# Performance work log

Hardware: AMD Instinct MI355X
Metric: run time of the kernel (lower is better)

Reference implementation:

```python
import jax, jax.numpy as jnp
import numpy as np

ATTN_MASK_VALUE = -1e10
N, D_IN, D_HEAD, D_OUT = 8192, 1024, 128, 1024


def setup_inputs() -> dict:
    key = jax.random.key(0)
    k_x, k_wqkv, k_bqkv, k_wo, k_bo = jax.random.split(key, 5)
    x = jax.random.normal(k_x, (N, D_IN), dtype=jnp.float32)
    # flax Dense default: lecun_normal kernel, zeros bias; use scaled normal for test
    w_qkv = jax.random.normal(k_wqkv, (D_IN, 3 * D_HEAD), dtype=jnp.float32) / np.sqrt(D_IN)
    b_qkv = jnp.zeros((3 * D_HEAD,), dtype=jnp.float32)
    w_out = jax.random.normal(k_wo, (D_HEAD, D_OUT), dtype=jnp.float32) / np.sqrt(D_HEAD)
    b_out = jnp.zeros((D_OUT,), dtype=jnp.float32)
    return {"x": x, "w_qkv": w_qkv, "b_qkv": b_qkv, "w_out": w_out, "b_out": b_out}


def reference(x, w_qkv, b_qkv, w_out, b_out):
    n = x.shape[0]
    scale = D_HEAD ** (-0.5)
    qkv = x @ w_qkv + b_qkv                      # [n, 3*dh]
    q, k, v = jnp.split(qkv, 3, axis=-1)         # each [n, dh]
    sim = jnp.einsum('id,jd->ij', q, k) * scale  # [n, n]
    mask = jnp.triu(jnp.ones((n, n), dtype=bool), 1)
    sim = jnp.where(mask, ATTN_MASK_VALUE, sim)
    attn = jax.nn.softmax(sim, axis=-1)
    out = jnp.einsum('ij,jd->id', attn, v)       # [n, dh]
    return out @ w_out + b_out                   # [n, d_out]
```

## Files before the change

kernel.cpp:

```cpp
#include <hip/hip_runtime.h>
#include <stdint.h>

typedef __attribute__((ext_vector_type(4))) float f32x4;
typedef __attribute__((ext_vector_type(8))) __bf16 bf16x8;

#define MFMA16(a, b, c) __builtin_amdgcn_mfma_f32_16x16x32_bf16(a, b, c, 0, 0, 0)
#define GLOAD16(g, l)                                                              \
  __builtin_amdgcn_global_load_lds(                                                \
      (const __attribute__((address_space(1))) unsigned int*)(g),                  \
      (__attribute__((address_space(3))) unsigned int*)(l), 16, 0, 0)
#define EXP2F(x) __builtin_amdgcn_exp2f(x)

static __device__ __forceinline__ unsigned short f2b(float f) {
  unsigned int u = __float_as_uint(f);
  u += 0x7fff + ((u >> 16) & 1);
  return (unsigned short)(u >> 16);
}
static __device__ __forceinline__ float b2f(unsigned short h) {
  unsigned int u = ((unsigned int)h) << 16;
  return __uint_as_float(u);
}
static __device__ __forceinline__ unsigned int cvt_pk_bf16(float a, float b) {
  unsigned int r;
  asm("v_cvt_pk_bf16_f32 %0, %1, %2" : "=v"(r) : "v"(a), "v"(b));
  return r;
}

#define NROWS 8192
#define DIN   1024
#define DH    128
#define DOUT  1024

__global__ void k_convert(const float* __restrict__ x, const float* __restrict__ wqkv,
                          const float* __restrict__ wout,
                          unsigned short* __restrict__ xb,
                          unsigned short* __restrict__ wqkvT, unsigned short* __restrict__ woutT) {
  const int bid = blockIdx.x;
  const int tid = threadIdx.x;
  if (bid < 8192) {
    int i = (bid * 256 + tid) * 4;
    float4 v = *reinterpret_cast<const float4*>(x + i);
    ushort4 h;
    h.x = f2b(v.x); h.y = f2b(v.y); h.z = f2b(v.z); h.w = f2b(v.w);
    *reinterpret_cast<ushort4*>(xb + i) = h;
    return;
  }
  __shared__ float t[64][65];
  const int wb = bid - 8192;
  const float* src;
  unsigned short* dst;
  int k0, n0, sstride, dstride;
  if (wb < 96) {
    int kt = wb / 6, nt = wb % 6;
    k0 = kt * 64; n0 = nt * 64;
    src = wqkv; sstride = 384; dst = wqkvT; dstride = 1024;
  } else {
    int b2 = wb - 96;
    int kt = b2 & 1, nt = b2 >> 1;
    k0 = kt * 64; n0 = nt * 64;
    src = wout; sstride = 1024; dst = woutT; dstride = 128;
  }
  const int r = tid >> 4, c4 = (tid & 15) * 4;
#pragma unroll
  for (int j = 0; j < 4; ++j) {
    int rr = r + j * 16;
    float4 v = *reinterpret_cast<const float4*>(src + (size_t)(k0 + rr) * sstride + n0 + c4);
    t[rr][c4 + 0] = v.x; t[rr][c4 + 1] = v.y; t[rr][c4 + 2] = v.z; t[rr][c4 + 3] = v.w;
  }
  __syncthreads();
#pragma unroll
  for (int j = 0; j < 4; ++j) {
    int rn = r + j * 16;
    ushort4 h;
    h.x = f2b(t[c4 + 0][rn]); h.y = f2b(t[c4 + 1][rn]);
    h.z = f2b(t[c4 + 2][rn]); h.w = f2b(t[c4 + 3][rn]);
    *reinterpret_cast<ushort4*>(dst + (size_t)(n0 + rn) * dstride + k0 + c4) = h;
  }
}

__launch_bounds__(256, 2)
__global__ void k_qkv_gemm(const unsigned short* __restrict__ xb, const unsigned short* __restrict__ wT,
                           const float* __restrict__ bqkv,
                           unsigned short* __restrict__ Qb, unsigned short* __restrict__ Kb,
                           unsigned short* __restrict__ Vb) {
  const int hb = blockIdx.x;
  const int xcd = hb & 7, jj = hb >> 3;
  const int tau = xcd * 48 + jj;
  const int bn = tau % 6, bm = tau / 6;
  const int tid = threadIdx.x;
  const int lane = tid & 63, w = tid >> 6;
  const int l15 = lane & 15, g = lane >> 4;
  const int wm = (w >> 1) * 64, wn = (w & 1) * 32;
  const int row0 = bm * 128, col0 = bn * 64;

  __shared__ __align__(16) char Ash[2][16384];
  __shared__ __align__(16) char Bsh[2][8192];

  f32x4 acc[4][2] = {};

#define QKV_STAGE(k0, buf)                                                          \
  {                                                                                 \
    _Pragma("unroll")                                                               \
    for (int j2 = 0; j2 < 4; ++j2) {                                                \
      int idx = j2 * 256 + tid;                                                     \
      int r = idx >> 3, gg = idx & 7, sgg = gg ^ (r & 7);                           \
      GLOAD16(xb + (size_t)(row0 + r) * DIN + (k0) + sgg * 8, Ash[buf] + idx * 16); \
    }                                                                               \
    _Pragma("unroll")                                                               \
    for (int j2 = 0; j2 < 2; ++j2) {                                                \
      int idx = j2 * 256 + tid;                                                     \
      int r = idx >> 3, gg = idx & 7, sgg = gg ^ (r & 7);                           \
      GLOAD16(wT + (size_t)(col0 + r) * DIN + (k0) + sgg * 8, Bsh[buf] + idx * 16); \
    }                                                                               \
  }

  QKV_STAGE(0, 0);
  __syncthreads();
  int cur = 0;
  for (int k0 = 0; k0 < DIN; k0 += 64) {
    if (k0 + 64 < DIN) QKV_STAGE(k0 + 64, cur ^ 1);
#pragma unroll
    for (int ksl = 0; ksl < 2; ++ksl) {
      bf16x8 af[4], bfr[2];
#pragma unroll
      for (int i = 0; i < 4; ++i) {
        int r = wm + i * 16 + l15;
        int ba = r * 128 + ksl * 64 + g * 16;
        af[i] = *reinterpret_cast<bf16x8*>(Ash[cur] + (ba ^ ((r & 7) << 4)));
      }
#pragma unroll
      for (int jn = 0; jn < 2; ++jn) {
        int n = wn + jn * 16 + l15;
        int bb = n * 128 + ksl * 64 + g * 16;
        bfr[jn] = *reinterpret_cast<bf16x8*>(Bsh[cur] + (bb ^ ((n & 7) << 4)));
      }
#pragma unroll
      for (int i = 0; i < 4; ++i)
#pragma unroll
        for (int jn = 0; jn < 2; ++jn)
          acc[i][jn] = MFMA16(af[i], bfr[jn], acc[i][jn]);
    }
    __syncthreads();
    cur ^= 1;
  }

  const int which = col0 >> 7;
  const int inner = col0 & 127;
  unsigned short* outb = (which == 0) ? Qb : (which == 1 ? Kb : Vb);
#pragma unroll
  for (int i = 0; i < 4; ++i)
#pragma unroll
    for (int jn = 0; jn < 2; ++jn)
#pragma unroll
      for (int r = 0; r < 4; ++r) {
        int grow = row0 + wm + i * 16 + g * 4 + r;
        int lcol = wn + jn * 16 + l15;
        float vv = acc[i][jn][r] + bqkv[col0 + lcol];
        outb[(size_t)grow * DH + inner + lcol] = f2b(vv);
      }
}

__global__ void k_transpose_v(const unsigned short* __restrict__ V, unsigned short* __restrict__ VT) {
  __shared__ __align__(16) unsigned short t[64 * 128];
  const int b = blockIdx.x;
  const int tid = threadIdx.x;
  const int kv0 = b * 64;
#pragma unroll
  for (int j = 0; j < 4; ++j) {
    int c = j * 256 + tid;
    int r = c >> 4, cc = (c & 15) * 8;
    uint4 v = *reinterpret_cast<const uint4*>(V + (size_t)(kv0 + r) * DH + cc);
    int col = (cc + ((r >> 3) & 7) * 8) & 127;
    *reinterpret_cast<uint4*>(&t[r * 128 + col]) = v;
  }
  __syncthreads();
#pragma unroll
  for (int j = 0; j < 4; ++j) {
    int c = j * 256 + tid;
    int d = c >> 3, kk = (c & 7) * 8;
    unsigned short tmp[8];
#pragma unroll
    for (int e = 0; e < 8; ++e) {
      int r = kk + e;
      int col = (d + ((r >> 3) & 7) * 8) & 127;
      tmp[e] = t[r * 128 + col];
    }
    *reinterpret_cast<uint4*>(VT + (size_t)d * NROWS + kv0 + kk) = *reinterpret_cast<uint4*>(tmp);
  }
}

__launch_bounds__(256, 2)
__global__ void k_flash(const unsigned short* __restrict__ Q, const unsigned short* __restrict__ Kg,
                        const unsigned short* __restrict__ VT,
                        unsigned short* __restrict__ Opart, float* __restrict__ MLpart, int LQ) {
  const int ci = blockIdx.x;
  const int t = (int)(gridDim.y - 1) - (int)blockIdx.y;
  const int Jq = 1 << LQ;
  if (ci * Jq > t) return;
  const int qb = t << 7;
  const int ks = ci * (Jq << 7);
  const int ke = min(ks + (Jq << 7), qb + 128);
  const int nsteps = (ke - ks) >> 6;

  const int a = t >> LQ, b = t & (Jq - 1);
  const int slot = t + ((Jq * a * (a - 1)) >> 1) + a * b + ci;

  const int tid = threadIdx.x;
  const int lane = tid & 63, w = tid >> 6;
  const int l15 = lane & 15, g = lane >> 4;

  __shared__ __align__(16) char Ksh[2][16384];
  __shared__ __align__(16) char Vsh[2][16384];
  __shared__ __align__(16) char Psh[4][4096];

  const int qr0 = qb + w * 16 + l15;
  const int qr1 = qr0 + 64;
  bf16x8 qf0[4], qf1[4];
#pragma unroll
  for (int d = 0; d < 4; ++d) {
    qf0[d] = *reinterpret_cast<const bf16x8*>(Q + (size_t)qr0 * DH + d * 32 + g * 8);
    qf1[d] = *reinterpret_cast<const bf16x8*>(Q + (size_t)qr1 * DH + d * 32 + g * 8);
  }

  f32x4 acco0[8] = {}, acco1[8] = {};
  float m0 = -1e30f, l0 = 0.f, m1 = -1e30f, l1 = 0.f;
  const float c2 = 0.08838834764831843f * 1.4426950408889634f;

#define FL_STAGE(kv0, buf)                                                            \
  {                                                                                   \
    _Pragma("unroll")                                                                 \
    for (int j2 = 0; j2 < 4; ++j2) {                                                  \
      int idx = j2 * 256 + tid;                                                       \
      int r = idx >> 4, gg = idx & 15, sgg = gg ^ (r & 7);                            \
      GLOAD16(Kg + (size_t)((kv0) + r) * DH + sgg * 8, Ksh[buf] + idx * 16);          \
    }                                                                                 \
    _Pragma("unroll")                                                                 \
    for (int j2 = 0; j2 < 4; ++j2) {                                                  \
      int idx = j2 * 256 + tid;                                                       \
      int d = idx >> 3, gg = idx & 7, sgg = gg ^ (d & 7);                             \
      GLOAD16(VT + (size_t)d * NROWS + (kv0) + sgg * 8, Vsh[buf] + idx * 16);         \
    }                                                                                 \
  }

  char* Pw = Psh[w];

  FL_STAGE(ks, 0);
  __syncthreads();
  int cur = 0;

  for (int s = 0; s < nsteps; ++s) {
    const int kv0 = ks + (s << 6);
    if (s + 1 < nsteps) FL_STAGE(kv0 + 64, cur ^ 1);
    const bool act0 = (kv0 < qb + 64);

    f32x4 accs0[4] = {}, accs1[4] = {};
    __builtin_amdgcn_s_setprio(1);
    if (act0) {
#pragma unroll
      for (int jc = 0; jc < 4; ++jc)
#pragma unroll
        for (int d = 0; d < 4; ++d) {
          int r = jc * 16 + l15;
          int byte = r * 256 + d * 64 + g * 16; byte ^= (r & 7) << 4;
          bf16x8 kf = *reinterpret_cast<bf16x8*>(Ksh[cur] + byte);
          accs1[jc] = MFMA16(kf, qf1[d], accs1[jc]);
          accs0[jc] = MFMA16(kf, qf0[d], accs0[jc]);
        }
    } else {
#pragma unroll
      for (int jc = 0; jc < 4; ++jc)
#pragma unroll
        for (int d = 0; d < 4; ++d) {
          int r = jc * 16 + l15;
          int byte = r * 256 + d * 64 + g * 16; byte ^= (r & 7) << 4;
          bf16x8 kf = *reinterpret_cast<bf16x8*>(Ksh[cur] + byte);
          accs1[jc] = MFMA16(kf, qf1[d], accs1[jc]);
        }
    }
    __builtin_amdgcn_s_setprio(0);

#define SOFTMAX_PW(ACCS, ACCO, M, L, QROW, ROWBASE)                                   \
    {                                                                                 \
      float p[4][4];                                                                  \
      float mx = -3e38f;                                                              \
      _Pragma("unroll")                                                               \
      for (int jc = 0; jc < 4; ++jc)                                                  \
        _Pragma("unroll")                                                             \
        for (int r = 0; r < 4; ++r) {                                                 \
          float sv = ACCS[jc][r] * c2;                                                \
          int kk = kv0 + jc * 16 + (g << 2) + r;                                      \
          sv = (kk <= (QROW)) ? sv : -3e38f;                                          \
          p[jc][r] = sv;                                                              \
          mx = fmaxf(mx, sv);                                                         \
        }                                                                             \
      mx = fmaxf(mx, __shfl_xor(mx, 16));                                             \
      mx = fmaxf(mx, __shfl_xor(mx, 32));                                             \
      if (!__all(mx <= M + 8.f)) {             \
        float mnew = fmaxf(M, mx);                                                    \
        float fac = EXP2F(M - mnew);                                                  \
        L *= fac;                                                                     \
        M = mnew;                                                                     \
        _Pragma("unroll")                                                             \
        for (int dc = 0; dc < 8; ++dc)                                                \
          _Pragma("unroll")                                                           \
          for (int r = 0; r < 4; ++r) ACCO[dc][r] *= fac;                             \
      }                                                                               \
      float ps = 0.f;                                                                 \
      _Pragma("unroll")                                                               \
      for (int jc = 0; jc < 4; ++jc)                                                  \
        _Pragma("unroll")                                                             \
        for (int r = 0; r < 4; ++r) {                                                 \
          float e = EXP2F(p[jc][r] - M);                                              \
          p[jc][r] = e; ps += e;                                                      \
        }                                                                             \
      ps += __shfl_xor(ps, 16);                                                       \
      ps += __shfl_xor(ps, 32);                                                       \
      L += ps;                                                                        \
      int rq = (ROWBASE) + l15;                                                       \
      _Pragma("unroll")                                                               \
      for (int jc = 0; jc < 4; ++jc) {                                                \
        uint2 pb;                                                                     \
        pb.x = cvt_pk_bf16(p[jc][0], p[jc][1]);                                       \
        pb.y = cvt_pk_bf16(p[jc][2], p[jc][3]);                                       \
        int byte = rq * 128 + jc * 32 + g * 8; byte ^= (rq & 7) << 4;                 \
        *reinterpret_cast<uint2*>(Pw + byte) = pb;                                    \
      }                                                                               \
    }

    if (act0) SOFTMAX_PW(accs0, acco0, m0, l0, qr0, 0);
    SOFTMAX_PW(accs1, acco1, m1, l1, qr1, 16);

    bf16x8 pf1[2];
#pragma unroll
    for (int ks2 = 0; ks2 < 2; ++ks2) {
      int rq = 16 + l15;
      int byte = rq * 128 + ks2 * 64 + g * 16; byte ^= (rq & 7) << 4;
      pf1[ks2] = *reinterpret_cast<bf16x8*>(Pw + byte);
    }
    __builtin_amdgcn_s_setprio(1);
    if (act0) {
      bf16x8 pf0[2];
#pragma unroll
      for (int ks2 = 0; ks2 < 2; ++ks2) {
        int byte = l15 * 128 + ks2 * 64 + g * 16; byte ^= (l15 & 7) << 4;
        pf0[ks2] = *reinterpret_cast<bf16x8*>(Pw + byte);
      }
#pragma unroll
      for (int dc = 0; dc < 8; ++dc) {
        int vr = dc * 16 + l15;
        int b0 = vr * 128 + g * 16; b0 ^= (vr & 7) << 4;
        bf16x8 vf0 = *reinterpret_cast<bf16x8*>(Vsh[cur] + b0);
        bf16x8 vf1 = *reinterpret_cast<bf16x8*>(Vsh[cur] + (b0 ^ 64));
        acco1[dc] = MFMA16(vf0, pf1[0], acco1[dc]);
        acco1[dc] = MFMA16(vf1, pf1[1], acco1[dc]);
        acco0[dc] = MFMA16(vf0, pf0[0], acco0[dc]);
        acco0[dc] = MFMA16(vf1, pf0[1], acco0[dc]);
      }
    } else {
#pragma unroll
      for (int dc = 0; dc < 8; ++dc) {
        int vr = dc * 16 + l15;
        int b0 = vr * 128 + g * 16; b0 ^= (vr & 7) << 4;
        bf16x8 vf0 = *reinterpret_cast<bf16x8*>(Vsh[cur] + b0);
        bf16x8 vf1 = *reinterpret_cast<bf16x8*>(Vsh[cur] + (b0 ^ 64));
        acco1[dc] = MFMA16(vf0, pf1[0], acco1[dc]);
        acco1[dc] = MFMA16(vf1, pf1[1], acco1[dc]);
      }
    }
    __builtin_amdgcn_s_setprio(0);
    __syncthreads();
    cur ^= 1;
  }

  const size_t r0 = (size_t)slot * 128 + w * 16 + l15;
  const size_t r1 = r0 + 64;
#pragma unroll
  for (int dc = 0; dc < 8; ++dc) {
    uint2 o0, o1;
    o0.x = cvt_pk_bf16(acco0[dc][0], acco0[dc][1]);
    o0.y = cvt_pk_bf16(acco0[dc][2], acco0[dc][3]);
    o1.x = cvt_pk_bf16(acco1[dc][0], acco1[dc][1]);
    o1.y = cvt_pk_bf16(acco1[dc][2], acco1[dc][3]);
    *reinterpret_cast<uint2*>(Opart + r0 * DH + dc * 16 + (g << 2)) = o0;
    *reinterpret_cast<uint2*>(Opart + r1 * DH + dc * 16 + (g << 2)) = o1;
  }
  if (g == 0) {
    MLpart[r0 * 2 + 0] = m0;
    MLpart[r0 * 2 + 1] = l0;
    MLpart[r1 * 2 + 0] = m1;
    MLpart[r1 * 2 + 1] = l1;
  }
}

__global__ void k_merge(const unsigned short* __restrict__ Opart, const float* __restrict__ MLpart,
                        unsigned short* __restrict__ O, int LQ) {
  int tg = blockIdx.x * 256 + threadIdx.x;
  int row = tg >> 5, d4 = (tg & 31) * 4;
  int t = row >> 7;
  int Jq = 1 << LQ;
  int a = t >> LQ, b = t & (Jq - 1);
  int base = t + ((Jq * a * (a - 1)) >> 1) + a * b;
  int nc = a + 1;
  int rowin = row & 127;
  float M = -3e38f;
  for (int i = 0; i < nc; ++i) M = fmaxf(M, MLpart[((size_t)(base + i) * 128 + rowin) * 2]);
  float L = 0.f;
  f32x4 acc = {};
  for (int i = 0; i < nc; ++i) {
    size_t sr = (size_t)(base + i) * 128 + rowin;
    float mi = MLpart[sr * 2];
    float li = MLpart[sr * 2 + 1];
    float wg = EXP2F(mi - M);
    L += li * wg;
    ushort4 o = *reinterpret_cast<const ushort4*>(Opart + sr * DH + d4);
    acc[0] += wg * b2f(o.x); acc[1] += wg * b2f(o.y);
    acc[2] += wg * b2f(o.z); acc[3] += wg * b2f(o.w);
  }
  float inv = 1.f / L;
  uint2 hv;
  hv.x = cvt_pk_bf16(acc[0] * inv, acc[1] * inv);
  hv.y = cvt_pk_bf16(acc[2] * inv, acc[3] * inv);
  *reinterpret_cast<uint2*>(O + (size_t)row * DH + d4) = hv;
}

__launch_bounds__(256, 2)
__global__ void k_out_gemm(const unsigned short* __restrict__ O, const unsigned short* __restrict__ wT,
                           const float* __restrict__ bout, float* __restrict__ out) {
  const int hb = blockIdx.x;
  const int xcd = hb & 7, jj = hb >> 3;
  const int tau = xcd * 64 + jj;
  const int bn = tau & 7, bm = tau >> 3;
  const int tid = threadIdx.x;
  const int lane = tid & 63, w = tid >> 6;
  const int l15 = lane & 15, g = lane >> 4;
  const int wm = (w >> 1) * 64, wn = (w & 1) * 64;
  const int row0 = bm * 128, col0 = bn * 128;

  __shared__ __align__(16) char Ash[2][16384];
  __shared__ __align__(16) char Bsh[2][16384];

  f32x4 acc[4][4] = {};

#define OUT_STAGE(k0, buf)                                                          \
  {                                                                                 \
    _Pragma("unroll")                                                               \
    for (int j2 = 0; j2 < 4; ++j2) {                                                \
      int idx = j2 * 256 + tid;                                                     \
      int r = idx >> 3, gg = idx & 7, sgg = gg ^ (r & 7);                           \
      GLOAD16(O + (size_t)(row0 + r) * DH + (k0) + sgg * 8, Ash[buf] + idx * 16);   \
      GLOAD16(wT + (size_t)(col0 + r) * DH + (k0) + sgg * 8, Bsh[buf] + idx * 16);  \
    }                                                                               \
  }

  OUT_STAGE(0, 0);
  __syncthreads();
  int cur = 0;
  for (int k0 = 0; k0 < DH; k0 += 64) {
    if (k0 + 64 < DH) OUT_STAGE(k0 + 64, cur ^ 1);
#pragma unroll
    for (int ksl = 0; ksl < 2; ++ksl) {
      bf16x8 af[4], bfr[4];
#pragma unroll
      for (int i = 0; i < 4; ++i) {
        int r = wm + i * 16 + l15;
        int ba = r * 128 + ksl * 64 + g * 16;
        af[i] = *reinterpret_cast<bf16x8*>(Ash[cur] + (ba ^ ((r & 7) << 4)));
        int n = wn + i * 16 + l15;
        int bb = n * 128 + ksl * 64 + g * 16;
        bfr[i] = *reinterpret_cast<bf16x8*>(Bsh[cur] + (bb ^ ((n & 7) << 4)));
      }
#pragma unroll
      for (int i = 0; i < 4; ++i)
#pragma unroll
        for (int jn = 0; jn < 4; ++jn)
          acc[i][jn] = MFMA16(af[i], bfr[jn], acc[i][jn]);
    }
    __syncthreads();
    cur ^= 1;
  }

#pragma unroll
  for (int i = 0; i < 4; ++i)
#pragma unroll
    for (int jn = 0; jn < 4; ++jn)
#pragma unroll
      for (int r = 0; r < 4; ++r) {
        int grow = row0 + wm + i * 16 + g * 4 + r;
        int gcol = col0 + wn + jn * 16 + l15;
        out[(size_t)grow * DOUT + gcol] = acc[i][jn][r] + bout[gcol];
      }
}

extern "C" void kernel_launch(void* const* d_in, const int* in_sizes, int n_in,
                              void* d_out, int out_size, void* d_ws, size_t ws_size,
                              hipStream_t stream) {
  const float* x    = (const float*)d_in[0];
  const float* wqkv = (const float*)d_in[1];
  const float* bqkv = (const float*)d_in[2];
  const float* wout = (const float*)d_in[3];
  const float* bout = (const float*)d_in[4];
  float* out = (float*)d_out;

  size_t fixed = 786432 + 262144 + (size_t)NROWS * DIN * 2 + (size_t)5 * NROWS * DH * 2;
  int LQ = 2;
  size_t slots = 0;
  for (; LQ <= 6; ++LQ) {
    int Jq = 1 << LQ, A = 64 / Jq;
    slots = (size_t)Jq * A * (A + 1) / 2;
    size_t need = fixed + slots * ((size_t)128 * DH * 2 + 128 * 8);
    if (need <= ws_size || LQ == 6) break;
  }

  char* ws = (char*)d_ws;
  size_t off = 0;
  unsigned short* wqkvT = (unsigned short*)(ws + off); off += (size_t)384 * 1024 * 2;
  unsigned short* woutT = (unsigned short*)(ws + off); off += (size_t)1024 * 128 * 2;
  unsigned short* xb  = (unsigned short*)(ws + off); off += (size_t)NROWS * DIN * 2;
  unsigned short* Qb  = (unsigned short*)(ws + off); off += (size_t)NROWS * DH * 2;
  unsigned short* Kb  = (unsigned short*)(ws + off); off += (size_t)NROWS * DH * 2;
  unsigned short* Vb  = (unsigned short*)(ws + off); off += (size_t)NROWS * DH * 2;
  unsigned short* VTb = (unsigned short*)(ws + off); off += (size_t)NROWS * DH * 2;
  unsigned short* Ob  = (unsigned short*)(ws + off); off += (size_t)NROWS * DH * 2;
  unsigned short* Opart = (unsigned short*)(ws + off); off += slots * (size_t)128 * DH * 2;
  float* MLpart = (float*)(ws + off); off += slots * (size_t)128 * 8;

  k_convert<<<8320, 256, 0, stream>>>(x, wqkv, wout, xb, wqkvT, woutT);
  k_qkv_gemm<<<384, 256, 0, stream>>>(xb, wqkvT, bqkv, Qb, Kb, Vb);
  k_transpose_v<<<128, 256, 0, stream>>>(Vb, VTb);
  k_flash<<<dim3(64 >> LQ, 64), 256, 0, stream>>>(Qb, Kb, VTb, Opart, MLpart, LQ);
  k_merge<<<(NROWS * 32) / 256, 256, 0, stream>>>(Opart, MLpart, Ob, LQ);
  k_out_gemm<<<512, 256, 0, stream>>>(Ob, woutT, bout, out);
}
```

Before: 110.8 us.

## Fuse x fp32-to-bf16 conversion and V transpose into QKV GEMM

```diff
diff --git a/kernel.cpp b/kernel.cpp
--- a/kernel.cpp
+++ b/kernel.cpp
@@ -31,35 +31,24 @@
 #define DH    128
 #define DOUT  1024
 
-__global__ void k_convert(const float* __restrict__ x, const float* __restrict__ wqkv,
-                          const float* __restrict__ wout,
-                          unsigned short* __restrict__ xb,
-                          unsigned short* __restrict__ wqkvT, unsigned short* __restrict__ woutT) {
+__global__ void k_convert_w(const float* __restrict__ wqkv, const float* __restrict__ wout,
+                            unsigned short* __restrict__ wqkvT, unsigned short* __restrict__ woutT) {
+  __shared__ float t[64][65];
   const int bid = blockIdx.x;
-  const int tid = threadIdx.x;
-  if (bid < 8192) {
-    int i = (bid * 256 + tid) * 4;
-    float4 v = *reinterpret_cast<const float4*>(x + i);
-    ushort4 h;
-    h.x = f2b(v.x); h.y = f2b(v.y); h.z = f2b(v.z); h.w = f2b(v.w);
-    *reinterpret_cast<ushort4*>(xb + i) = h;
-    return;
-  }
-  __shared__ float t[64][65];
-  const int wb = bid - 8192;
   const float* src;
   unsigned short* dst;
   int k0, n0, sstride, dstride;
-  if (wb < 96) {
-    int kt = wb / 6, nt = wb % 6;
+  if (bid < 96) {
+    int kt = bid / 6, nt = bid % 6;
     k0 = kt * 64; n0 = nt * 64;
     src = wqkv; sstride = 384; dst = wqkvT; dstride = 1024;
   } else {
-    int b2 = wb - 96;
+    int b2 = bid - 96;
     int kt = b2 & 1, nt = b2 >> 1;
     k0 = kt * 64; n0 = nt * 64;
     src = wout; sstride = 1024; dst = woutT; dstride = 128;
   }
+  const int tid = threadIdx.x;
   const int r = tid >> 4, c4 = (tid & 15) * 4;
 #pragma unroll
   for (int j = 0; j < 4; ++j) {
@@ -79,10 +68,10 @@
 }
 
 __launch_bounds__(256, 2)
-__global__ void k_qkv_gemm(const unsigned short* __restrict__ xb, const unsigned short* __restrict__ wT,
+__global__ void k_qkv_gemm(const float* __restrict__ x, const unsigned short* __restrict__ wT,
                            const float* __restrict__ bqkv,
                            unsigned short* __restrict__ Qb, unsigned short* __restrict__ Kb,
-                           unsigned short* __restrict__ Vb) {
+                           unsigned short* __restrict__ VT) {
   const int hb = blockIdx.x;
   const int xcd = hb & 7, jj = hb >> 3;
   const int tau = xcd * 48 + jj;
@@ -103,8 +92,15 @@
     _Pragma("unroll")                                                               \
     for (int j2 = 0; j2 < 4; ++j2) {                                                \
       int idx = j2 * 256 + tid;                                                     \
-      int r = idx >> 3, gg = idx & 7, sgg = gg ^ (r & 7);                           \
-      GLOAD16(xb + (size_t)(row0 + r) * DIN + (k0) + sgg * 8, Ash[buf] + idx * 16); \
+      int r = idx >> 3, gg = idx & 7;                                               \
+      const float* sp = x + (size_t)(row0 + r) * DIN + (k0) + gg * 8;               \
+      float4 v0 = *reinterpret_cast<const float4*>(sp);                             \
+      float4 v1 = *reinterpret_cast<const float4*>(sp + 4);                         \
+      uint4 h;                                                                      \
+      h.x = cvt_pk_bf16(v0.x, v0.y); h.y = cvt_pk_bf16(v0.z, v0.w);                 \
+      h.z = cvt_pk_bf16(v1.x, v1.y); h.w = cvt_pk_bf16(v1.z, v1.w);                 \
+      int db = (r * 128 + gg * 16) ^ ((r & 7) << 4);                                \
+      *reinterpret_cast<uint4*>(Ash[buf] + db) = h;                                 \
     }                                                                               \
     _Pragma("unroll")                                                               \
     for (int j2 = 0; j2 < 2; ++j2) {                                                \
@@ -146,46 +142,33 @@
 
   const int which = col0 >> 7;
   const int inner = col0 & 127;
-  unsigned short* outb = (which == 0) ? Qb : (which == 1 ? Kb : Vb);
-#pragma unroll
-  for (int i = 0; i < 4; ++i)
-#pragma unroll
-    for (int jn = 0; jn < 2; ++jn)
-#pragma unroll
-      for (int r = 0; r < 4; ++r) {
-        int grow = row0 + wm + i * 16 + g * 4 + r;
+  if (which == 2) {
+#pragma unroll
+    for (int i = 0; i < 4; ++i)
+#pragma unroll
+      for (int jn = 0; jn < 2; ++jn) {
         int lcol = wn + jn * 16 + l15;
-        float vv = acc[i][jn][r] + bqkv[col0 + lcol];
-        outb[(size_t)grow * DH + inner + lcol] = f2b(vv);
-      }
-}
-
-__global__ void k_transpose_v(const unsigned short* __restrict__ V, unsigned short* __restrict__ VT) {
-  __shared__ __align__(16) unsigned short t[64 * 128];
-  const int b = blockIdx.x;
-  const int tid = threadIdx.x;
-  const int kv0 = b * 64;
-#pragma unroll
-  for (int j = 0; j < 4; ++j) {
-    int c = j * 256 + tid;
-    int r = c >> 4, cc = (c & 15) * 8;
-    uint4 v = *reinterpret_cast<const uint4*>(V + (size_t)(kv0 + r) * DH + cc);
-    int col = (cc + ((r >> 3) & 7) * 8) & 127;
-    *reinterpret_cast<uint4*>(&t[r * 128 + col]) = v;
-  }
-  __syncthreads();
-#pragma unroll
-  for (int j = 0; j < 4; ++j) {
-    int c = j * 256 + tid;
-    int d = c >> 3, kk = (c & 7) * 8;
-    unsigned short tmp[8];
-#pragma unroll
-    for (int e = 0; e < 8; ++e) {
-      int r = kk + e;
-      int col = (d + ((r >> 3) & 7) * 8) & 127;
-      tmp[e] = t[r * 128 + col];
-    }
-    *reinterpret_cast<uint4*>(VT + (size_t)d * NROWS + kv0 + kk) = *reinterpret_cast<uint4*>(tmp);
+        int d = inner + lcol;
+        float bias = bqkv[col0 + lcol];
+        int kvb = row0 + wm + i * 16 + g * 4;
+        ushort4 o;
+        o.x = f2b(acc[i][jn][0] + bias); o.y = f2b(acc[i][jn][1] + bias);
+        o.z = f2b(acc[i][jn][2] + bias); o.w = f2b(acc[i][jn][3] + bias);
+        *reinterpret_cast<ushort4*>(VT + (size_t)d * NROWS + kvb) = o;
+      }
+  } else {
+    unsigned short* outb = (which == 0) ? Qb : Kb;
+#pragma unroll
+    for (int i = 0; i < 4; ++i)
+#pragma unroll
+      for (int jn = 0; jn < 2; ++jn)
+#pragma unroll
+        for (int r = 0; r < 4; ++r) {
+          int grow = row0 + wm + i * 16 + g * 4 + r;
+          int lcol = wn + jn * 16 + l15;
+          float vv = acc[i][jn][r] + bqkv[col0 + lcol];
+          outb[(size_t)grow * DH + inner + lcol] = f2b(vv);
+        }
   }
 }
 
@@ -501,7 +484,7 @@
   const float* bout = (const float*)d_in[4];
   float* out = (float*)d_out;
 
-  size_t fixed = 786432 + 262144 + (size_t)NROWS * DIN * 2 + (size_t)5 * NROWS * DH * 2;
+  size_t fixed = 786432 + 262144 + (size_t)4 * NROWS * DH * 2;
   int LQ = 2;
   size_t slots = 0;
   for (; LQ <= 6; ++LQ) {
@@ -515,18 +498,15 @@
   size_t off = 0;
   unsigned short* wqkvT = (unsigned short*)(ws + off); off += (size_t)384 * 1024 * 2;
   unsigned short* woutT = (unsigned short*)(ws + off); off += (size_t)1024 * 128 * 2;
-  unsigned short* xb  = (unsigned short*)(ws + off); off += (size_t)NROWS * DIN * 2;
   unsigned short* Qb  = (unsigned short*)(ws + off); off += (size_t)NROWS * DH * 2;
   unsigned short* Kb  = (unsigned short*)(ws + off); off += (size_t)NROWS * DH * 2;
-  unsigned short* Vb  = (unsigned short*)(ws + off); off += (size_t)NROWS * DH * 2;
   unsigned short* VTb = (unsigned short*)(ws + off); off += (size_t)NROWS * DH * 2;
   unsigned short* Ob  = (unsigned short*)(ws + off); off += (size_t)NROWS * DH * 2;
   unsigned short* Opart = (unsigned short*)(ws + off); off += slots * (size_t)128 * DH * 2;
   float* MLpart = (float*)(ws + off); off += slots * (size_t)128 * 8;
 
-  k_convert<<<8320, 256, 0, stream>>>(x, wqkv, wout, xb, wqkvT, woutT);
-  k_qkv_gemm<<<384, 256, 0, stream>>>(xb, wqkvT, bqkv, Qb, Kb, Vb);
-  k_transpose_v<<<128, 256, 0, stream>>>(Vb, VTb);
+  k_convert_w<<<128, 256, 0, stream>>>(wqkv, wout, wqkvT, woutT);
+  k_qkv_gemm<<<384, 256, 0, stream>>>(x, wqkvT, bqkv, Qb, Kb, VTb);
   k_flash<<<dim3(64 >> LQ, 64), 256, 0, stream>>>(Qb, Kb, VTb, Opart, MLpart, LQ);
   k_merge<<<(NROWS * 32) / 256, 256, 0, stream>>>(Opart, MLpart, Ob, LQ);
   k_out_gemm<<<512, 256, 0, stream>>>(Ob, woutT, bout, out);
```

Measured after the change: 111.0 us. No clear change (+0.2%).
